# Optimization experiments

Hardware: AMD Instinct MI355X
Metric: run time of the kernel (lower is better)

Reference implementation:

```python
import jax, jax.numpy as jnp
import numpy as np

EMBED_DIM = 1024
NUM_HEADS = 16
HEAD_DIM = EMBED_DIM // NUM_HEADS


def setup_inputs() -> dict:
    key = jax.random.key(0)
    k1, k2, k3, k4, k5 = jax.random.split(key, 5)
    B, S, D = 2, 2048, EMBED_DIM
    s_in = 1.0 / np.sqrt(D)
    x = jax.random.normal(k1, (B, S, D), dtype=jnp.float32)
    W_qkv = jax.random.uniform(k2, (D, 3 * D), dtype=jnp.float32, minval=-s_in, maxval=s_in)
    b_qkv = jax.random.uniform(k3, (3 * D,), dtype=jnp.float32, minval=-s_in, maxval=s_in)
    W_out = jax.random.uniform(k4, (D, D), dtype=jnp.float32, minval=-s_in, maxval=s_in)
    b_out = jax.random.uniform(k5, (D,), dtype=jnp.float32, minval=-s_in, maxval=s_in)
    return {"x": x, "W_qkv": W_qkv, "b_qkv": b_qkv, "W_out": W_out, "b_out": b_out}


def reference(x, W_qkv, b_qkv, W_out, b_out):
    B, S, D = x.shape
    H, Hd = NUM_HEADS, HEAD_DIM
    qkv = x @ W_qkv + b_qkv                      # [B,S,3D]
    qkv = qkv.reshape(B, S, 3, H, Hd)
    q = qkv[:, :, 0].transpose(0, 2, 1, 3)       # [B,H,S,Hd]
    k = qkv[:, :, 1].transpose(0, 2, 1, 3)
    v = qkv[:, :, 2].transpose(0, 2, 1, 3)
    scores = jnp.einsum('bhsd,bhtd->bhst', q, k) / jnp.sqrt(jnp.float32(Hd))
    attn = jax.nn.softmax(scores, axis=-1)       # dropout is identity in eval mode
    out = jnp.einsum('bhst,bhtd->bhsd', attn, v)
    out = out.transpose(0, 2, 1, 3).reshape(B, S, D)
    return out @ W_out + b_out
```

## Files before the change

kernel.cpp:

```cpp
#include <hip/hip_runtime.h>
#include <stdint.h>
#include <math.h>

#define EMBED 1024
#define HEADS 16
#define HDIM  64
#define SEQ   2048
#define BATCH 2

typedef __bf16 bf16x8 __attribute__((ext_vector_type(8)));
typedef float  f32x4  __attribute__((ext_vector_type(4)));
typedef unsigned short u16x8 __attribute__((ext_vector_type(8)));
typedef unsigned short u16x4 __attribute__((ext_vector_type(4)));
typedef uint32_t u32x4v __attribute__((ext_vector_type(4)));

static __device__ __forceinline__ unsigned short f2bf(float f){
  union { float f; uint32_t u; } v; v.f = f;
  uint32_t u = v.u;
  uint32_t r = (u + 0x7FFFu + ((u >> 16) & 1u)) >> 16;
  return (unsigned short)r;
}
static __device__ __forceinline__ bf16x8 as_bf(u16x8 v){ return __builtin_bit_cast(bf16x8, v); }

static __device__ __forceinline__ uint32_t pk_bf16(float a, float b){
#if defined(__has_builtin) && __has_builtin(__builtin_amdgcn_cvt_pk_bf16_f32)
  typedef __bf16 bf16x2 __attribute__((ext_vector_type(2)));
  bf16x2 p = __builtin_amdgcn_cvt_pk_bf16_f32(a, b);
  return __builtin_bit_cast(uint32_t, p);
#else
  return (uint32_t)f2bf(a) | ((uint32_t)f2bf(b) << 16);
#endif
}

static __device__ __forceinline__ float fexp2(float x){
#if defined(__has_builtin) && __has_builtin(__builtin_amdgcn_exp2f)
  return __builtin_amdgcn_exp2f(x);
#else
  return exp2f(x);
#endif
}

static __device__ __forceinline__ void stage16(const unsigned short* gp,
                                               unsigned short* lp_wave, int lane){
#if defined(__has_builtin) && __has_builtin(__builtin_amdgcn_global_load_lds)
  __builtin_amdgcn_global_load_lds((const __attribute__((address_space(1))) void*)gp,
                                   (__attribute__((address_space(3))) void*)lp_wave,
                                   16, 0, 0);
#else
  *(u16x8*)(lp_wave + lane * 8) = *(const u16x8*)gp;
#endif
}

__global__ __launch_bounds__(256) void prep(
    const float* __restrict__ x,      unsigned short* __restrict__ xb,
    const float* __restrict__ W_qkv,  unsigned short* __restrict__ wqkvT,
    const float* __restrict__ W_out,  unsigned short* __restrict__ woutT)
{
  __shared__ unsigned short T[32 * 36];
  const int bid = blockIdx.x;
  const int t   = threadIdx.x;

  if (bid < 4096){
    int i = (bid * 256 + t) * 4;
    float4 v = *(const float4*)(x + i);
    u16x4 o;
    o[0] = f2bf(v.x); o[1] = f2bf(v.y); o[2] = f2bf(v.z); o[3] = f2bf(v.w);
    *(u16x4*)(xb + i) = o;
    return;
  }
  const float* W; unsigned short* Wt; int N, n0, k0;
  if (bid < 7168){
    int idx = bid - 4096;
    W = W_qkv; Wt = wqkvT; N = 3072;
    n0 = (idx % 96) * 32; k0 = (idx / 96) * 32;
  } else {
    int idx = bid - 7168;
    W = W_out; Wt = woutT; N = 1024;
    n0 = (idx & 31) * 32; k0 = (idx >> 5) * 32;
  }
  int kr = t >> 3, nc = (t & 7) * 4;
  float4 wv = *(const float4*)(W + (size_t)(k0 + kr) * N + n0 + nc);
  T[(nc + 0) * 36 + kr] = f2bf(wv.x);
  T[(nc + 1) * 36 + kr] = f2bf(wv.y);
  T[(nc + 2) * 36 + kr] = f2bf(wv.z);
  T[(nc + 3) * 36 + kr] = f2bf(wv.w);
  __syncthreads();
  int nr = t >> 3, kc = (t & 7) * 4;
  *(u16x4*)(Wt + (size_t)(n0 + nr) * 1024 + k0 + kc) = *(const u16x4*)&T[nr * 36 + kc];
}

__global__ __launch_bounds__(256, 6) void gemm_qkv(
    const unsigned short* __restrict__ A,
    const unsigned short* __restrict__ Bt,
    const float* __restrict__ bias,
    unsigned short* __restrict__ q_ws,
    unsigned short* __restrict__ k_ws,
    unsigned short* __restrict__ vt_ws,
    int M, int N, int K)
{
  __shared__ unsigned short SM[12288];
  unsigned short* As = SM;
  unsigned short* Bs = SM + 8192;
  const int tid  = threadIdx.x;
  const int bm   = blockIdx.x, bn = blockIdx.y;
  const int w    = tid >> 6, lane = tid & 63;
  const int quad = lane >> 4, l16 = lane & 15;
  const int wm   = (w >> 1) * 64, wn = (w & 1) * 32;

  f32x4 acc[4][2] = {};

  for (int k0 = 0; k0 < 1024; k0 += 64) {
    #pragma unroll
    for (int i = 0; i < 4; i++){
      int c = w * 4 + i;
      int row = c * 8 + (lane >> 3);
      int kg = (lane & 7) ^ (row & 7);
      stage16(A + (size_t)(bm * 128 + row) * 1024 + k0 + kg * 8, As + c * 512, lane);
    }
    #pragma unroll
    for (int i = 0; i < 2; i++){
      int c = w * 2 + i;
      int row = c * 8 + (lane >> 3);
      int kg = (lane & 7) ^ (row & 7);
      stage16(Bt + (size_t)(bn * 64 + row) * 1024 + k0 + kg * 8, Bs + c * 512, lane);
    }
    __syncthreads();

    #pragma unroll
    for (int kk = 0; kk < 2; kk++){
      bf16x8 af[4], bfr[2];
      #pragma unroll
      for (int t = 0; t < 4; t++){
        int ra = wm + t * 16 + l16;
        af[t] = as_bf(*(const u16x8*)&As[(ra << 6) + ((((kk << 2) + quad) ^ (ra & 7)) << 3)]);
      }
      #pragma unroll
      for (int t = 0; t < 2; t++){
        int rb = wn + t * 16 + l16;
        bfr[t] = as_bf(*(const u16x8*)&Bs[(rb << 6) + ((((kk << 2) + quad) ^ (rb & 7)) << 3)]);
      }
      #pragma unroll
      for (int mt = 0; mt < 4; mt++)
        #pragma unroll
        for (int nt = 0; nt < 2; nt++)
          acc[mt][nt] = __builtin_amdgcn_mfma_f32_16x16x32_bf16(af[mt], bfr[nt], acc[mt][nt], 0, 0, 0);
    }
    __syncthreads();
  }

  const int which = (bn * 64) >> 10;
  const int b = bm >> 4;
  const int S0 = (bm & 15) * 128;

  if (which == 2){
    #pragma unroll
    for (int nt = 0; nt < 2; nt++){
      int coln = wn + nt * 16 + l16;
      float bv = bias[bn * 64 + coln];
      #pragma unroll
      for (int mt = 0; mt < 4; mt++){
        int sposl = wm + (mt >> 1) * 32 + quad * 8 + (mt & 1) * 4;
        #pragma unroll
        for (int r = 0; r < 4; r++)
          SM[coln * 136 + sposl + r] = f2bf(acc[mt][nt][r] + bv);
      }
    }
    __syncthreads();
    const int h = bn - 32;
    unsigned short* vp = vt_ws + (size_t)(b * HEADS + h) * SEQ * HDIM;
    #pragma unroll
    for (int p = 0; p < 4; p++){
      int idx = p * 256 + tid;
      int nl = idx >> 4;
      int s0 = (idx & 15) * 8;
      u16x8 v = *(const u16x8*)&SM[nl * 136 + s0];
      *(u16x8*)(vp + (size_t)nl * SEQ + S0 + s0) = v;
    }
  } else {
    const float scale = (which == 0) ? 0.18033688f : 1.0f;
    #pragma unroll
    for (int nt = 0; nt < 2; nt++){
      int coln = wn + nt * 16 + l16;
      float bv = bias[bn * 64 + coln];
      #pragma unroll
      for (int mt = 0; mt < 4; mt++){
        int sl = wm + mt * 16 + quad * 4;
        #pragma unroll
        for (int r = 0; r < 4; r++)
          SM[(sl + r) * 72 + coln] = f2bf((acc[mt][nt][r] + bv) * scale);
      }
    }
    __syncthreads();
    const int h = (which == 0) ? bn : (bn - 16);
    unsigned short* dst = ((which == 0) ? q_ws : k_ws) + (size_t)(b * HEADS + h) * SEQ * HDIM;
    #pragma unroll
    for (int p = 0; p < 4; p++){
      int idx = p * 256 + tid;
      int sl = idx >> 3;
      int c0 = (idx & 7) * 8;
      u16x8 v = *(const u16x8*)&SM[sl * 72 + c0];
      *(u16x8*)(dst + (size_t)(S0 + sl) * HDIM + c0) = v;
    }
  }
}

__global__ __launch_bounds__(256) void gemm_out(
    const unsigned short* __restrict__ A,
    const unsigned short* __restrict__ Bt,
    const float* __restrict__ bias,
    float* __restrict__ Cout,
    int M, int N, int K)
{
  __shared__ unsigned short SM[17408];
  unsigned short* As = SM;
  unsigned short* Bs = SM + 8192;
  const int tid  = threadIdx.x;
  const int bm   = blockIdx.x, bn = blockIdx.y;
  const int w    = tid >> 6, lane = tid & 63;
  const int quad = lane >> 4, l16 = lane & 15;
  const int wm   = (w >> 1) * 64, wn = (w & 1) * 32;

  f32x4 acc[4][2] = {};

  for (int k0 = 0; k0 < K; k0 += 64) {
    #pragma unroll
    for (int i = 0; i < 4; i++){
      int c = w * 4 + i;
      int row = c * 8 + (lane >> 3);
      int kg = (lane & 7) ^ (row & 7);
      stage16(A + (size_t)(bm * 128 + row) * K + k0 + kg * 8, As + c * 512, lane);
    }
    #pragma unroll
    for (int i = 0; i < 2; i++){
      int c = w * 2 + i;
      int row = c * 8 + (lane >> 3);
      int kg = (lane & 7) ^ (row & 7);
      stage16(Bt + (size_t)(bn * 64 + row) * K + k0 + kg * 8, Bs + c * 512, lane);
    }
    __syncthreads();

    #pragma unroll
    for (int kk = 0; kk < 2; kk++){
      bf16x8 af[4], bfr[2];
      #pragma unroll
      for (int t = 0; t < 4; t++){
        int ra = wm + t * 16 + l16;
        af[t] = as_bf(*(const u16x8*)&As[(ra << 6) + ((((kk << 2) + quad) ^ (ra & 7)) << 3)]);
      }
      #pragma unroll
      for (int t = 0; t < 2; t++){
        int rb = wn + t * 16 + l16;
        bfr[t] = as_bf(*(const u16x8*)&Bs[(rb << 6) + ((((kk << 2) + quad) ^ (rb & 7)) << 3)]);
      }
      #pragma unroll
      for (int mt = 0; mt < 4; mt++)
        #pragma unroll
        for (int nt = 0; nt < 2; nt++)
          acc[mt][nt] = __builtin_amdgcn_mfma_f32_16x16x32_bf16(af[mt], bfr[nt], acc[mt][nt], 0, 0, 0);
    }
    __syncthreads();
  }

  float* F = (float*)SM;
  #pragma unroll
  for (int nt = 0; nt < 2; nt++){
    int coln = wn + nt * 16 + l16;
    float bv = bias[bn * 64 + coln];
    #pragma unroll
    for (int mt = 0; mt < 4; mt++){
      int rowl = wm + mt * 16 + quad * 4;
      #pragma unroll
      for (int r = 0; r < 4; r++)
        F[(rowl + r) * 66 + coln] = acc[mt][nt][r] + bv;
    }
  }
  __syncthreads();

  #pragma unroll
  for (int p = 0; p < 8; p++){
    int idx  = p * 256 + tid;
    int rowl = idx >> 4;
    int c4   = (idx & 15) * 4;
    float4 v = *(const float4*)&F[rowl * 66 + c4];
    *(float4*)(Cout + (size_t)(bm * 128 + rowl) * N + bn * 64 + c4) = v;
  }
}

__global__ __launch_bounds__(512, 1) void attn(
    const unsigned short* __restrict__ q_ws,
    const unsigned short* __restrict__ k_ws,
    const unsigned short* __restrict__ vt_ws,
    unsigned short* __restrict__ o_ws)
{
  __shared__ unsigned short Qs[256 * 64];
  __shared__ unsigned short Ks[2][64 * 64];
  __shared__ unsigned short VTs[2][64 * 64];
  const int tid  = threadIdx.x;
  const int wgid = blockIdx.x;
  const int lin  = (wgid & 7) * 32 + (wgid >> 3);
  const int bh   = lin >> 3, qt = lin & 7;
  const int w    = tid >> 6, lane = tid & 63;
  const int quad = lane >> 4, l16 = lane & 15;
  const size_t base = (size_t)bh * SEQ * HDIM;

  #pragma unroll
  for (int i = 0; i < 4; i++){
    int c = w * 4 + i;
    int row = c * 8 + (lane >> 3);
    int kg = (lane & 7) ^ (row & 7);
    stage16(q_ws + base + (size_t)(qt * 256 + row) * HDIM + kg * 8, &Qs[c * 512], lane);
  }

  const int srow = w * 8 + (lane >> 3);
  const int skg  = (lane & 7) ^ (srow & 7);
  const int dofs = w * 512 + lane * 8;

  stage16(k_ws  + base + (size_t)srow * HDIM + skg * 8, &Ks[0][w * 512],  lane);
  stage16(vt_ws + base + (size_t)srow * SEQ + skg * 8,  &VTs[0][w * 512], lane);
  __syncthreads();

  bf16x8 bq[2][2];
  #pragma unroll
  for (int mq = 0; mq < 2; mq++){
    int row = w * 32 + mq * 16 + l16;
    #pragma unroll
    for (int ks = 0; ks < 2; ks++)
      bq[mq][ks] = as_bf(*(const u16x8*)&Qs[(row << 6) + ((((ks << 2) + quad) ^ (row & 7)) << 3)]);
  }

  const unsigned short* kp = k_ws  + base + (size_t)(64 + srow) * HDIM + skg * 8;
  const unsigned short* vp = vt_ws + base + (size_t)srow * SEQ + 64 + skg * 8;

  const bool grpB = (w >= 4);

  f32x4 acc[2][4] = {};
  float li[2] = {0.f, 0.f};
  f32x4 sf[4][2];
  bf16x8 bvB[2][4];

  for (int kt = 0; kt < SEQ / 64; kt++){
    const int cur = kt & 1;
    const int co  = cur * 4096;
    u16x8 kpre, vpre;
    if (kt < SEQ / 64 - 1){
      kpre = *(const u16x8*)kp;  kp += 64 * HDIM;
      vpre = *(const u16x8*)vp;  vp += 64;
    }

    if (!grpB){
      f32x4 sa[4][2] = {};
      #pragma unroll
      for (int ks = 0; ks < 2; ks++)
        #pragma unroll
        for (int nt = 0; nt < 4; nt++){
          int rk = nt * 16 + l16;
          bf16x8 ak = as_bf(*(const u16x8*)&Ks[0][co + (rk << 6) + ((((ks << 2) + quad) ^ (rk & 7)) << 3)]);
          #pragma unroll
          for (int mq = 0; mq < 2; mq++)
            sa[nt][mq] = __builtin_amdgcn_mfma_f32_16x16x32_bf16(ak, bq[mq][ks], sa[nt][mq], 0, 0, 0);
        }

      #pragma unroll
      for (int nt = 0; nt < 4; nt++)
        #pragma unroll
        for (int mq = 0; mq < 2; mq++)
          #pragma unroll
          for (int r = 0; r < 4; r++)
            sa[nt][mq][r] = fexp2(sa[nt][mq][r]);
      #pragma unroll
      for (int mq = 0; mq < 2; mq++)
        #pragma unroll
        for (int nt = 0; nt < 4; nt++)
          li[mq] += (sa[nt][mq][0] + sa[nt][mq][1]) + (sa[nt][mq][2] + sa[nt][mq][3]);

      #pragma unroll
      for (int c = 0; c < 2; c++){
        bf16x8 ap[2];
        #pragma unroll
        for (int mq = 0; mq < 2; mq++){
          u32x4v aw;
          aw[0] = pk_bf16(sa[c * 2][mq][0],     sa[c * 2][mq][1]);
          aw[1] = pk_bf16(sa[c * 2][mq][2],     sa[c * 2][mq][3]);
          aw[2] = pk_bf16(sa[c * 2 + 1][mq][0], sa[c * 2 + 1][mq][1]);
          aw[3] = pk_bf16(sa[c * 2 + 1][mq][2], sa[c * 2 + 1][mq][3]);
          ap[mq] = __builtin_bit_cast(bf16x8, aw);
        }
        #pragma unroll
        for (int nt = 0; nt < 4; nt++){
          int rv = nt * 16 + l16;
          bf16x8 bv = as_bf(*(const u16x8*)&VTs[0][co + (rv << 6) + ((((c << 2) + quad) ^ (rv & 7)) << 3)]);
          #pragma unroll
          for (int mq = 0; mq < 2; mq++)
            acc[mq][nt] = __builtin_amdgcn_mfma_f32_16x16x32_bf16(ap[mq], bv, acc[mq][nt], 0, 0, 0);
        }
      }
    } else {
      if (kt > 0){
        #pragma unroll
        for (int nt = 0; nt < 4; nt++)
          #pragma unroll
          for (int mq = 0; mq < 2; mq++)
            #pragma unroll
            for (int r = 0; r < 4; r++)
              sf[nt][mq][r] = fexp2(sf[nt][mq][r]);
        #pragma unroll
        for (int mq = 0; mq < 2; mq++)
          #pragma unroll
          for (int nt = 0; nt < 4; nt++)
            li[mq] += (sf[nt][mq][0] + sf[nt][mq][1]) + (sf[nt][mq][2] + sf[nt][mq][3]);

        #pragma unroll
        for (int c = 0; c < 2; c++){
          bf16x8 ap[2];
          #pragma unroll
          for (int mq = 0; mq < 2; mq++){
            u32x4v aw;
            aw[0] = pk_bf16(sf[c * 2][mq][0],     sf[c * 2][mq][1]);
            aw[1] = pk_bf16(sf[c * 2][mq][2],     sf[c * 2][mq][3]);
            aw[2] = pk_bf16(sf[c * 2 + 1][mq][0], sf[c * 2 + 1][mq][1]);
            aw[3] = pk_bf16(sf[c * 2 + 1][mq][2], sf[c * 2 + 1][mq][3]);
            ap[mq] = __builtin_bit_cast(bf16x8, aw);
          }
          #pragma unroll
          for (int nt = 0; nt < 4; nt++)
            #pragma unroll
            for (int mq = 0; mq < 2; mq++)
              acc[mq][nt] = __builtin_amdgcn_mfma_f32_16x16x32_bf16(ap[mq], bvB[c][nt], acc[mq][nt], 0, 0, 0);
        }
      }

      #pragma unroll
      for (int nt = 0; nt < 4; nt++)
        #pragma unroll
        for (int mq = 0; mq < 2; mq++)
          sf[nt][mq] = f32x4{0.f, 0.f, 0.f, 0.f};
      #pragma unroll
      for (int ks = 0; ks < 2; ks++)
        #pragma unroll
        for (int nt = 0; nt < 4; nt++){
          int rk = nt * 16 + l16;
          bf16x8 ak = as_bf(*(const u16x8*)&Ks[0][co + (rk << 6) + ((((ks << 2) + quad) ^ (rk & 7)) << 3)]);
          #pragma unroll
          for (int mq = 0; mq < 2; mq++)
            sf[nt][mq] = __builtin_amdgcn_mfma_f32_16x16x32_bf16(ak, bq[mq][ks], sf[nt][mq], 0, 0, 0);
        }

      #pragma unroll
      for (int c = 0; c < 2; c++)
        #pragma unroll
        for (int nt = 0; nt < 4; nt++){
          int rv = nt * 16 + l16;
          bvB[c][nt] = as_bf(*(const u16x8*)&VTs[0][co + (rv << 6) + ((((c << 2) + quad) ^ (rv & 7)) << 3)]);
        }
    }

    if (kt < SEQ / 64 - 1){
      const int no = co ^ 4096;
      *(u16x8*)&Ks[0][no + dofs]  = kpre;
      *(u16x8*)&VTs[0][no + dofs] = vpre;
    }
    __syncthreads();
  }

  if (grpB){
    #pragma unroll
    for (int nt = 0; nt < 4; nt++)
      #pragma unroll
      for (int mq = 0; mq < 2; mq++)
        #pragma unroll
        for (int r = 0; r < 4; r++)
          sf[nt][mq][r] = fexp2(sf[nt][mq][r]);
    #pragma unroll
    for (int mq = 0; mq < 2; mq++)
      #pragma unroll
      for (int nt = 0; nt < 4; nt++)
        li[mq] += (sf[nt][mq][0] + sf[nt][mq][1]) + (sf[nt][mq][2] + sf[nt][mq][3]);
    #pragma unroll
    for (int c = 0; c < 2; c++){
      bf16x8 ap[2];
      #pragma unroll
      for (int mq = 0; mq < 2; mq++){
        u32x4v aw;
        aw[0] = pk_bf16(sf[c * 2][mq][0],     sf[c * 2][mq][1]);
        aw[1] = pk_bf16(sf[c * 2][mq][2],     sf[c * 2][mq][3]);
        aw[2] = pk_bf16(sf[c * 2 + 1][mq][0], sf[c * 2 + 1][mq][1]);
        aw[3] = pk_bf16(sf[c * 2 + 1][mq][2], sf[c * 2 + 1][mq][3]);
        ap[mq] = __builtin_bit_cast(bf16x8, aw);
      }
      #pragma unroll
      for (int nt = 0; nt < 4; nt++)
        #pragma unroll
        for (int mq = 0; mq < 2; mq++)
          acc[mq][nt] = __builtin_amdgcn_mfma_f32_16x16x32_bf16(ap[mq], bvB[c][nt], acc[mq][nt], 0, 0, 0);
    }
  }

  #pragma unroll
  for (int mq = 0; mq < 2; mq++){
    li[mq] += __shfl_xor(li[mq], 16);
    li[mq] += __shfl_xor(li[mq], 32);
  }
  float inv[2] = {1.0f / li[0], 1.0f / li[1]};
  float invr[2][4];
  #pragma unroll
  for (int mq = 0; mq < 2; mq++)
    #pragma unroll
    for (int r = 0; r < 4; r++)
      invr[mq][r] = __shfl(inv[mq], quad * 4 + r);

  int b = bh >> 4, h = bh & 15;
  #pragma unroll
  for (int mq = 0; mq < 2; mq++)
    #pragma unroll
    for (int nt = 0; nt < 4; nt++)
      #pragma unroll
      for (int r = 0; r < 4; r++){
        int s = qt * 256 + w * 32 + mq * 16 + quad * 4 + r;
        int d = h * 64 + nt * 16 + l16;
        o_ws[((size_t)(b * SEQ + s)) * EMBED + d] = f2bf(acc[mq][nt][r] * invr[mq][r]);
      }
}

extern "C" void kernel_launch(void* const* d_in, const int* in_sizes, int n_in,
                              void* d_out, int out_size, void* d_ws, size_t ws_size,
                              hipStream_t stream) {
  const float* x     = (const float*)d_in[0];
  const float* W_qkv = (const float*)d_in[1];
  const float* b_qkv = (const float*)d_in[2];
  const float* W_out = (const float*)d_in[3];
  const float* b_out = (const float*)d_in[4];
  float* out = (float*)d_out;

  char* ws = (char*)d_ws;
  unsigned short* xb    = (unsigned short*)(ws);
  unsigned short* o     = (unsigned short*)(ws);
  unsigned short* q     = (unsigned short*)(ws + ((size_t)8  << 20));
  unsigned short* k     = (unsigned short*)(ws + ((size_t)16 << 20));
  unsigned short* vt    = (unsigned short*)(ws + ((size_t)24 << 20));
  unsigned short* wqkvT = (unsigned short*)(ws + ((size_t)32 << 20));
  unsigned short* woutT = (unsigned short*)(ws + ((size_t)38 << 20));

  prep<<<dim3(8192), dim3(256), 0, stream>>>(x, xb, W_qkv, wqkvT, W_out, woutT);

  gemm_qkv<<<dim3(32, 48), dim3(256), 0, stream>>>(
      xb, wqkvT, b_qkv, q, k, vt, 4096, 3072, 1024);

  attn<<<dim3(256), dim3(512), 0, stream>>>(q, k, vt, o);

  gemm_out<<<dim3(32, 16), dim3(256), 0, stream>>>(
      o, woutT, b_out, out, 4096, 1024, 1024);
}
```

Baseline: 187.7 us.

## Restructure attention into 2-wave blocks with per-wave async K/V staging

The attention kernel moves from 512-thread blocks, where 8 waves shared K/V tiles and were split into two ping-pong groups, to 128-thread blocks of 2 waves. Each wave owns 64 query rows and its own double-buffered K/V LDS region, staged by direct-to-LDS loads and synchronised with s_waitcnt instead of __syncthreads. Q fragments are loaded straight from global memory into registers. This removes block-wide barriers and the group split, but each wave now loads K/V separately, so global and LDS traffic per query rises, and the larger accumulator tiles raise register pressure.

Result: slower. 203.0 us (+8.2%).

```diff
diff --git a/kernel.cpp b/kernel.cpp
--- a/kernel.cpp
+++ b/kernel.cpp
@@ -286,236 +286,133 @@
   }
 }
 
-__global__ __launch_bounds__(512, 1) void attn(
+__global__ __launch_bounds__(128, 1) void attn(
     const unsigned short* __restrict__ q_ws,
     const unsigned short* __restrict__ k_ws,
     const unsigned short* __restrict__ vt_ws,
     unsigned short* __restrict__ o_ws)
 {
-  __shared__ unsigned short Qs[256 * 64];
-  __shared__ unsigned short Ks[2][64 * 64];
-  __shared__ unsigned short VTs[2][64 * 64];
+  __shared__ unsigned short SM[32768];
   const int tid  = threadIdx.x;
   const int wgid = blockIdx.x;
-  const int lin  = (wgid & 7) * 32 + (wgid >> 3);
-  const int bh   = lin >> 3, qt = lin & 7;
+  const int lin  = (wgid & 7) * 64 + (wgid >> 3);
+  const int bh   = lin >> 4, qt = lin & 15;
   const int w    = tid >> 6, lane = tid & 63;
   const int quad = lane >> 4, l16 = lane & 15;
   const size_t base = (size_t)bh * SEQ * HDIM;
-
-  #pragma unroll
-  for (int i = 0; i < 4; i++){
-    int c = w * 4 + i;
-    int row = c * 8 + (lane >> 3);
-    int kg = (lane & 7) ^ (row & 7);
-    stage16(q_ws + base + (size_t)(qt * 256 + row) * HDIM + kg * 8, &Qs[c * 512], lane);
-  }
-
-  const int srow = w * 8 + (lane >> 3);
-  const int skg  = (lane & 7) ^ (srow & 7);
-  const int dofs = w * 512 + lane * 8;
-
-  stage16(k_ws  + base + (size_t)srow * HDIM + skg * 8, &Ks[0][w * 512],  lane);
-  stage16(vt_ws + base + (size_t)srow * SEQ + skg * 8,  &VTs[0][w * 512], lane);
-  __syncthreads();
-
-  bf16x8 bq[2][2];
-  #pragma unroll
-  for (int mq = 0; mq < 2; mq++){
-    int row = w * 32 + mq * 16 + l16;
+  unsigned short* Kb = SM + w * 16384;
+  unsigned short* Vb = Kb + 8192;
+  const int qrow0 = qt * 128 + w * 64;
+
+  bf16x8 bq[4][2];
+  #pragma unroll
+  for (int mq = 0; mq < 4; mq++)
     #pragma unroll
     for (int ks = 0; ks < 2; ks++)
-      bq[mq][ks] = as_bf(*(const u16x8*)&Qs[(row << 6) + ((((ks << 2) + quad) ^ (row & 7)) << 3)]);
-  }
-
-  const unsigned short* kp = k_ws  + base + (size_t)(64 + srow) * HDIM + skg * 8;
-  const unsigned short* vp = vt_ws + base + (size_t)srow * SEQ + 64 + skg * 8;
-
-  const bool grpB = (w >= 4);
-
-  f32x4 acc[2][4] = {};
-  float li[2] = {0.f, 0.f};
-  f32x4 sf[4][2];
-  bf16x8 bvB[2][4];
-
+      bq[mq][ks] = as_bf(*(const u16x8*)(q_ws + base +
+                     (size_t)(qrow0 + mq * 16 + l16) * HDIM + (ks * 4 + quad) * 8));
+
+  const int r8 = lane >> 3;
+  const int kg = (lane & 7) ^ r8;
+
+  #pragma unroll
+  for (int c = 0; c < 8; c++)
+    stage16(k_ws + base + (size_t)(c * 8 + r8) * HDIM + kg * 8, Kb + c * 512, lane);
+  #pragma unroll
+  for (int c = 0; c < 8; c++)
+    stage16(vt_ws + base + (size_t)(c * 8 + r8) * SEQ + kg * 8, Vb + c * 512, lane);
+
+  f32x4 acc[4][4] = {};
+  float li[4] = {0.f, 0.f, 0.f, 0.f};
+
+  #pragma unroll 1
   for (int kt = 0; kt < SEQ / 64; kt++){
-    const int cur = kt & 1;
-    const int co  = cur * 4096;
-    u16x8 kpre, vpre;
+    const int co = (kt & 1) * 4096;
+
     if (kt < SEQ / 64 - 1){
-      kpre = *(const u16x8*)kp;  kp += 64 * HDIM;
-      vpre = *(const u16x8*)vp;  vp += 64;
-    }
-
-    if (!grpB){
-      f32x4 sa[4][2] = {};
-      #pragma unroll
-      for (int ks = 0; ks < 2; ks++)
-        #pragma unroll
-        for (int nt = 0; nt < 4; nt++){
-          int rk = nt * 16 + l16;
-          bf16x8 ak = as_bf(*(const u16x8*)&Ks[0][co + (rk << 6) + ((((ks << 2) + quad) ^ (rk & 7)) << 3)]);
-          #pragma unroll
-          for (int mq = 0; mq < 2; mq++)
-            sa[nt][mq] = __builtin_amdgcn_mfma_f32_16x16x32_bf16(ak, bq[mq][ks], sa[nt][mq], 0, 0, 0);
-        }
-
-      #pragma unroll
-      for (int nt = 0; nt < 4; nt++)
-        #pragma unroll
-        for (int mq = 0; mq < 2; mq++)
-          #pragma unroll
-          for (int r = 0; r < 4; r++)
-            sa[nt][mq][r] = fexp2(sa[nt][mq][r]);
-      #pragma unroll
-      for (int mq = 0; mq < 2; mq++)
-        #pragma unroll
-        for (int nt = 0; nt < 4; nt++)
-          li[mq] += (sa[nt][mq][0] + sa[nt][mq][1]) + (sa[nt][mq][2] + sa[nt][mq][3]);
-
-      #pragma unroll
-      for (int c = 0; c < 2; c++){
-        bf16x8 ap[2];
-        #pragma unroll
-        for (int mq = 0; mq < 2; mq++){
-          u32x4v aw;
-          aw[0] = pk_bf16(sa[c * 2][mq][0],     sa[c * 2][mq][1]);
-          aw[1] = pk_bf16(sa[c * 2][mq][2],     sa[c * 2][mq][3]);
-          aw[2] = pk_bf16(sa[c * 2 + 1][mq][0], sa[c * 2 + 1][mq][1]);
-          aw[3] = pk_bf16(sa[c * 2 + 1][mq][2], sa[c * 2 + 1][mq][3]);
-          ap[mq] = __builtin_bit_cast(bf16x8, aw);
-        }
-        #pragma unroll
-        for (int nt = 0; nt < 4; nt++){
-          int rv = nt * 16 + l16;
-          bf16x8 bv = as_bf(*(const u16x8*)&VTs[0][co + (rv << 6) + ((((c << 2) + quad) ^ (rv & 7)) << 3)]);
-          #pragma unroll
-          for (int mq = 0; mq < 2; mq++)
-            acc[mq][nt] = __builtin_amdgcn_mfma_f32_16x16x32_bf16(ap[mq], bv, acc[mq][nt], 0, 0, 0);
-        }
-      }
+      const int no = ((kt + 1) & 1) * 4096;
+      const size_t krow = (size_t)((kt + 1) * 64);
+      #pragma unroll
+      for (int c = 0; c < 8; c++)
+        stage16(k_ws + base + (krow + c * 8 + r8) * HDIM + kg * 8, Kb + no + c * 512, lane);
+      #pragma unroll
+      for (int c = 0; c < 8; c++)
+        stage16(vt_ws + base + (size_t)(c * 8 + r8) * SEQ + krow + kg * 8, Vb + no + c * 512, lane);
+      asm volatile("s_waitcnt vmcnt(16)" ::: "memory");
     } else {
-      if (kt > 0){
-        #pragma unroll
-        for (int nt = 0; nt < 4; nt++)
-          #pragma unroll
-          for (int mq = 0; mq < 2; mq++)
-            #pragma unroll
-            for (int r = 0; r < 4; r++)
-              sf[nt][mq][r] = fexp2(sf[nt][mq][r]);
-        #pragma unroll
-        for (int mq = 0; mq < 2; mq++)
-          #pragma unroll
-          for (int nt = 0; nt < 4; nt++)
-            li[mq] += (sf[nt][mq][0] + sf[nt][mq][1]) + (sf[nt][mq][2] + sf[nt][mq][3]);
-
-        #pragma unroll
-        for (int c = 0; c < 2; c++){
-          bf16x8 ap[2];
-          #pragma unroll
-          for (int mq = 0; mq < 2; mq++){
-            u32x4v aw;
-            aw[0] = pk_bf16(sf[c * 2][mq][0],     sf[c * 2][mq][1]);
-            aw[1] = pk_bf16(sf[c * 2][mq][2],     sf[c * 2][mq][3]);
-            aw[2] = pk_bf16(sf[c * 2 + 1][mq][0], sf[c * 2 + 1][mq][1]);
-            aw[3] = pk_bf16(sf[c * 2 + 1][mq][2], sf[c * 2 + 1][mq][3]);
-            ap[mq] = __builtin_bit_cast(bf16x8, aw);
-          }
-          #pragma unroll
-          for (int nt = 0; nt < 4; nt++)
-            #pragma unroll
-            for (int mq = 0; mq < 2; mq++)
-              acc[mq][nt] = __builtin_amdgcn_mfma_f32_16x16x32_bf16(ap[mq], bvB[c][nt], acc[mq][nt], 0, 0, 0);
-        }
-      }
-
-      #pragma unroll
-      for (int nt = 0; nt < 4; nt++)
-        #pragma unroll
-        for (int mq = 0; mq < 2; mq++)
-          sf[nt][mq] = f32x4{0.f, 0.f, 0.f, 0.f};
-      #pragma unroll
-      for (int ks = 0; ks < 2; ks++)
-        #pragma unroll
-        for (int nt = 0; nt < 4; nt++){
-          int rk = nt * 16 + l16;
-          bf16x8 ak = as_bf(*(const u16x8*)&Ks[0][co + (rk << 6) + ((((ks << 2) + quad) ^ (rk & 7)) << 3)]);
-          #pragma unroll
-          for (int mq = 0; mq < 2; mq++)
-            sf[nt][mq] = __builtin_amdgcn_mfma_f32_16x16x32_bf16(ak, bq[mq][ks], sf[nt][mq], 0, 0, 0);
-        }
-
-      #pragma unroll
-      for (int c = 0; c < 2; c++)
-        #pragma unroll
-        for (int nt = 0; nt < 4; nt++){
-          int rv = nt * 16 + l16;
-          bvB[c][nt] = as_bf(*(const u16x8*)&VTs[0][co + (rv << 6) + ((((c << 2) + quad) ^ (rv & 7)) << 3)]);
-        }
-    }
-
-    if (kt < SEQ / 64 - 1){
-      const int no = co ^ 4096;
-      *(u16x8*)&Ks[0][no + dofs]  = kpre;
-      *(u16x8*)&VTs[0][no + dofs] = vpre;
-    }
-    __syncthreads();
-  }
-
-  if (grpB){
+      asm volatile("s_waitcnt vmcnt(0)" ::: "memory");
+    }
+
+    f32x4 sf[4][4] = {};
+    #pragma unroll
+    for (int ks = 0; ks < 2; ks++)
+      #pragma unroll
+      for (int nt = 0; nt < 4; nt++){
+        int rk = nt * 16 + l16;
+        bf16x8 ak = as_bf(*(const u16x8*)&Kb[co + (rk << 6) + ((((ks << 2) + quad) ^ (rk & 7)) << 3)]);
+        #pragma unroll
+        for (int mq = 0; mq < 4; mq++)
+          sf[nt][mq] = __builtin_amdgcn_mfma_f32_16x16x32_bf16(ak, bq[mq][ks], sf[nt][mq], 0, 0, 0);
+      }
+
     #pragma unroll
     for (int nt = 0; nt < 4; nt++)
       #pragma unroll
-      for (int mq = 0; mq < 2; mq++)
+      for (int mq = 0; mq < 4; mq++)
         #pragma unroll
         for (int r = 0; r < 4; r++)
           sf[nt][mq][r] = fexp2(sf[nt][mq][r]);
     #pragma unroll
-    for (int mq = 0; mq < 2; mq++)
+    for (int mq = 0; mq < 4; mq++)
       #pragma unroll
       for (int nt = 0; nt < 4; nt++)
         li[mq] += (sf[nt][mq][0] + sf[nt][mq][1]) + (sf[nt][mq][2] + sf[nt][mq][3]);
-    #pragma unroll
-    for (int c = 0; c < 2; c++){
-      bf16x8 ap[2];
-      #pragma unroll
-      for (int mq = 0; mq < 2; mq++){
+
+    #pragma unroll
+    for (int c2 = 0; c2 < 2; c2++){
+      bf16x8 ap[4];
+      #pragma unroll
+      for (int mq = 0; mq < 4; mq++){
         u32x4v aw;
-        aw[0] = pk_bf16(sf[c * 2][mq][0],     sf[c * 2][mq][1]);
-        aw[1] = pk_bf16(sf[c * 2][mq][2],     sf[c * 2][mq][3]);
-        aw[2] = pk_bf16(sf[c * 2 + 1][mq][0], sf[c * 2 + 1][mq][1]);
-        aw[3] = pk_bf16(sf[c * 2 + 1][mq][2], sf[c * 2 + 1][mq][3]);
+        aw[0] = pk_bf16(sf[c2 * 2][mq][0],     sf[c2 * 2][mq][1]);
+        aw[1] = pk_bf16(sf[c2 * 2][mq][2],     sf[c2 * 2][mq][3]);
+        aw[2] = pk_bf16(sf[c2 * 2 + 1][mq][0], sf[c2 * 2 + 1][mq][1]);
+        aw[3] = pk_bf16(sf[c2 * 2 + 1][mq][2], sf[c2 * 2 + 1][mq][3]);
         ap[mq] = __builtin_bit_cast(bf16x8, aw);
       }
       #pragma unroll
-      for (int nt = 0; nt < 4; nt++)
-        #pragma unroll
-        for (int mq = 0; mq < 2; mq++)
-          acc[mq][nt] = __builtin_amdgcn_mfma_f32_16x16x32_bf16(ap[mq], bvB[c][nt], acc[mq][nt], 0, 0, 0);
-    }
-  }
-
-  #pragma unroll
-  for (int mq = 0; mq < 2; mq++){
+      for (int nt = 0; nt < 4; nt++){
+        int rv = nt * 16 + l16;
+        bf16x8 bv = as_bf(*(const u16x8*)&Vb[co + (rv << 6) + ((((c2 << 2) + quad) ^ (rv & 7)) << 3)]);
+        #pragma unroll
+        for (int mq = 0; mq < 4; mq++)
+          acc[mq][nt] = __builtin_amdgcn_mfma_f32_16x16x32_bf16(ap[mq], bv, acc[mq][nt], 0, 0, 0);
+      }
+    }
+  }
+
+  #pragma unroll
+  for (int mq = 0; mq < 4; mq++){
     li[mq] += __shfl_xor(li[mq], 16);
     li[mq] += __shfl_xor(li[mq], 32);
   }
-  float inv[2] = {1.0f / li[0], 1.0f / li[1]};
-  float invr[2][4];
-  #pragma unroll
-  for (int mq = 0; mq < 2; mq++)
+  float inv[4], invr[4][4];
+  #pragma unroll
+  for (int mq = 0; mq < 4; mq++) inv[mq] = 1.0f / li[mq];
+  #pragma unroll
+  for (int mq = 0; mq < 4; mq++)
     #pragma unroll
     for (int r = 0; r < 4; r++)
       invr[mq][r] = __shfl(inv[mq], quad * 4 + r);
 
   int b = bh >> 4, h = bh & 15;
   #pragma unroll
-  for (int mq = 0; mq < 2; mq++)
+  for (int mq = 0; mq < 4; mq++)
     #pragma unroll
     for (int nt = 0; nt < 4; nt++)
       #pragma unroll
       for (int r = 0; r < 4; r++){
-        int s = qt * 256 + w * 32 + mq * 16 + quad * 4 + r;
+        int s = qrow0 + mq * 16 + quad * 4 + r;
         int d = h * 64 + nt * 16 + l16;
         o_ws[((size_t)(b * SEQ + s)) * EMBED + d] = f2bf(acc[mq][nt][r] * invr[mq][r]);
       }
@@ -545,7 +442,7 @@
   gemm_qkv<<<dim3(32, 48), dim3(256), 0, stream>>>(
       xb, wqkvT, b_qkv, q, k, vt, 4096, 3072, 1024);
 
-  attn<<<dim3(256), dim3(512), 0, stream>>>(q, k, vt, o);
+  attn<<<dim3(512), dim3(128), 0, stream>>>(q, k, vt, o);
 
   gemm_out<<<dim3(32, 16), dim3(256), 0, stream>>>(
       o, woutT, b_out, out, 4096, 1024, 1024);
```
